# Kernel tuning notes

Hardware: AMD Instinct MI355X
Metric: run time of the kernel (lower is better)

## Reference

```python
import jax, jax.numpy as jnp
import numpy as np
import math

B, H, L, DK, D, LOCAL = 4, 8, 2048, 64, 512, 4


def setup_inputs() -> dict:
    key = jax.random.key(0)
    ks = jax.random.split(key, 9)
    n = L
    return {
        'query': jax.random.normal(ks[0], (B, H, L, DK), jnp.float32),
        'key': jax.random.normal(ks[1], (B, H, L, DK), jnp.float32),
        'value': jax.random.normal(ks[2], (B, H, L, DK), jnp.float32),
        'users': jax.random.normal(ks[3], (B, L, D), jnp.float32),
        'mask': jnp.tril(jnp.ones((L, L), dtype=bool))[None, None],  # causal [1,1,L,L]
        'rel_pos_w': jax.random.normal(ks[4], (2 * n - 1, DK * LOCAL), jnp.float32) * 0.02,
        'user_proj_w': jax.random.normal(ks[5], (DK * LOCAL, D), jnp.float32) * 0.02,
        'user_proj_b': jax.random.normal(ks[6], (DK * LOCAL,), jnp.float32) * 0.02,
        'mlp_w': jax.random.normal(ks[7], (LOCAL, DK), jnp.float32) * 0.1,
        'mlp_b': jax.random.normal(ks[8], (LOCAL,), jnp.float32) * 0.1,
    }


def reference(query, key, value, users, mask, rel_pos_w, user_proj_w, user_proj_b, mlp_w, mlp_b):
    b, h, l, dk = query.shape
    local = mlp_w.shape[0]
    g = h - local
    n = l
    scale = 1.0 / math.sqrt(dk)
    NEG = -1e12  # MAX_VAL in the torch source

    # ---- global heads: plain softmax attention ----
    qg, kg, vg = query[:, :g], key[:, :g], value[:, :g]
    sg = jnp.einsum('bhqd,bhkd->bhqk', qg, kg) * scale
    sg = jnp.where(mask, sg, NEG)
    pg = jax.nn.softmax(sg, axis=-1)
    og = jnp.einsum('bhqk,bhkd->bhqd', pg, vg)

    # ---- local (LOCKER) heads ----
    ql, kl, vl = query[:, g:], key[:, g:], value[:, g:]
    sl = jnp.einsum('bhqd,bhkd->bhqk', ql, kl) * scale

    # reweight = Linear(d_k,1)(rel_pos + v_q + v_k + user_proj(users)_q) per local head.
    # Linear over a sum decomposes exactly (same math, avoids [b,local,l,l,dk] tensor):
    rel_tab = rel_pos_w.reshape(2 * n - 1, local, dk)
    rel_scores = jnp.einsum('rhd,hd->rh', rel_tab, mlp_w)          # [2n-1, local]
    pos = jnp.arange(n)
    distance = pos[None, :] - pos[:, None] + n - 1                  # [l, l]
    rel_term = rel_scores[distance].transpose(2, 0, 1)              # [local, l, l]

    v_term = jnp.einsum('bhkd,hd->bhk', vl, mlp_w)                  # [b, local, l]
    u = (users @ user_proj_w.T + user_proj_b).reshape(b, l, local, dk)
    u_term = jnp.einsum('bqhd,hd->bhq', u, mlp_w)                   # [b, local, l]

    reweight = (rel_term[None]
                + v_term[:, :, None, :]      # value_l.unsqueeze(-3): varies over key idx
                + v_term[:, :, :, None]      # value_l.unsqueeze(-2): varies over query idx
                + u_term[:, :, :, None]      # user term broadcast over key idx
                + mlp_b[None, :, None, None])

    sl = sl + reweight
    sl = jnp.where(mask, sl, NEG)
    pl = jax.nn.softmax(sl, axis=-1)
    ol = jnp.einsum('bhqk,bhkd->bhqd', pl, vl)

    return jnp.concatenate([og, ol], axis=1)  # [b, h, l, d_k]
```

## Files before the change

kernel.cpp:

```cpp
#include <hip/hip_runtime.h>

#define TL 2048
#define NHEAD 8
#define NLOC 4
#define L2E 1.44269504f
#define PSTRIDE 4352

typedef __attribute__((ext_vector_type(4))) float f32x4;
typedef __attribute__((ext_vector_type(16))) float f32x16;
typedef __attribute__((ext_vector_type(8))) __bf16 bf16x8;
typedef __attribute__((ext_vector_type(8))) unsigned short u16x8;
typedef __attribute__((ext_vector_type(4))) unsigned int u32x4;

static __device__ __forceinline__ unsigned short f2bf(float f) {
    unsigned u = __float_as_uint(f);
    u = (u + 0x7FFFu + ((u >> 16) & 1u)) >> 16;
    return (unsigned short)u;
}
static __device__ __forceinline__ unsigned int cvtpk(float a, float b) {
    unsigned int w;
    asm("v_cvt_pk_bf16_f32 %0, %1, %2" : "=v"(w) : "v"(a), "v"(b));
    return w;
}
static __device__ __forceinline__ void gl_lds16(const void* g, void* l) {
    __builtin_amdgcn_global_load_lds(
        (const __attribute__((address_space(1))) void*)g,
        (__attribute__((address_space(3))) void*)l, 16, 0, 0);
}

__global__ __launch_bounds__(256) void relscore_kernel(
    const float* __restrict__ rel_pos_w, const float* __restrict__ mlp_w,
    float* __restrict__ rel_sf) {
    int r = blockIdx.x;
    int t = threadIdx.x;
    int w = t >> 6, lane = t & 63;
    float v = rel_pos_w[r * 256 + t] * mlp_w[t];
#pragma unroll
    for (int off = 32; off; off >>= 1) v += __shfl_xor(v, off);
    if (lane == 0) rel_sf[w * 4096 + r] = v * L2E;
}

__global__ __launch_bounds__(256) void preconv_kernel(
    const float* __restrict__ key, const float* __restrict__ value,
    const float* __restrict__ mlp_w,
    unsigned short* __restrict__ Kb, unsigned short* __restrict__ Vtb,
    float* __restrict__ vtbf) {
    __shared__ float Vf[64][66];
    int blk = blockIdx.x;
    int t = threadIdx.x;
    int bh = blk >> 5, kt = blk & 31;
    int h = bh & 7, b = bh >> 3;
    size_t src = (size_t)blk * 4096;
    size_t dst = (size_t)blk * 4096;

#pragma unroll
    for (int i = 0; i < 2; ++i) {
        int ch = t + i * 256;
        int row = ch >> 3, c = ch & 7;
        const float* kp = key + src + row * 64 + c * 8;
        f32x4 a = *(const f32x4*)kp;
        f32x4 bb = *(const f32x4*)(kp + 4);
        u16x8 o;
#pragma unroll
        for (int j = 0; j < 4; ++j) { o[j] = f2bf(a[j]); o[4 + j] = f2bf(bb[j]); }
        *(u16x8*)&Kb[dst + row * 64 + ((c ^ (row & 7)) << 3)] = o;
    }
    {
        int row = t >> 2, q4 = t & 3;
        const float* vp = value + src + row * 64 + q4 * 16;
#pragma unroll
        for (int j = 0; j < 4; ++j)
            *(f32x4*)&Vf[row][q4 * 16 + j * 4] = *(const f32x4*)(vp + j * 4);
    }
    __syncthreads();
#pragma unroll
    for (int i = 0; i < 2; ++i) {
        int ch = t + i * 256;
        int dr = ch >> 3, c = ch & 7;
        u16x8 o;
#pragma unroll
        for (int j = 0; j < 8; ++j) o[j] = f2bf(Vf[c * 8 + j][dr]);
        *(u16x8*)&Vtb[dst + dr * 64 + ((c ^ (dr & 7)) << 3)] = o;
    }
    if (h >= NLOC) {
        int wave = t >> 6, lane = t & 63;
        float mw = mlp_w[(h - NLOC) * 64 + lane];
        float* vout = vtbf + (size_t)((b * NLOC + h - NLOC) * TL) + kt * 64;
#pragma unroll
        for (int i = 0; i < 16; ++i) {
            int row = wave * 16 + i;
            float v = Vf[row][lane] * mw;
#pragma unroll
            for (int off = 32; off; off >>= 1) v += __shfl_xor(v, off);
            if (lane == 0) vout[row] = v * L2E;
        }
    }
}

#define MFMA32(A, B, C) __builtin_amdgcn_mfma_f32_32x32x16_bf16(A, B, C, 0, 0, 0)

__global__ __launch_bounds__(256, 4) void attn_kernel(
    const float* __restrict__ query,
    const unsigned short* __restrict__ Kb, const unsigned short* __restrict__ Vtb,
    const float* __restrict__ rel_sf, const float* __restrict__ vtbf,
    float* __restrict__ part) {

    __shared__ __align__(16) unsigned char smem[35328];
    unsigned short* Ks0 = (unsigned short*)smem;
    unsigned short* Vt0 = (unsigned short*)(smem + 16384);
    float* relw  = (float*)(smem + 32768);
    float* biasf = (float*)(smem + 34816);

    int bid = blockIdx.x;
    int bh = bid & 31;
    int sid = bid >> 5;
    int i = 0, s = 0, acc = 0;
#pragma unroll
    for (int ii = 15; ii >= 0; --ii) {
        int ns = (2 * ii + 7) / 6;
        if (sid >= acc && sid < acc + ns) { i = ii; s = sid - acc; }
        acc += ns;
    }
    int k_b = 6 * s;
    int k_e = min(6 * s + 6, 2 * i + 2);
    int q0 = i << 7;

    int h = bh & 7, b = bh >> 3;
    bool islocal = (h >= NLOC);
    int t = threadIdx.x;
    int w = t >> 6;
    int l31 = t & 31;
    int hi = (t >> 5) & 1;
    int sw = l31 & 7;
    int qrel = 32 * w + l31;
    int qglob = q0 + qrel;
    int qmaxw = q0 + 32 * w + 31;

    size_t tbase = (size_t)bh * 32 * 4096;
    const unsigned short* Ktiles = Kb + tbase;
    const unsigned short* Vtiles = Vtb + tbase;
    const float* vtpf = vtbf + (islocal ? (size_t)((b * NLOC + h - NLOC) * TL) : 0);
    int idxlo = 64 * k_b - q0 + 1920;
    const float* relsrc = rel_sf + (islocal ? ((h - NLOC) * 4096 + idxlo) : 0);

    gl_lds16(Ktiles + (size_t)k_b * 4096 + t * 8, Ks0 + t * 8);
    gl_lds16(Ktiles + (size_t)k_b * 4096 + 2048 + t * 8, Ks0 + 2048 + t * 8);
    gl_lds16(Vtiles + (size_t)k_b * 4096 + t * 8, Vt0 + t * 8);
    gl_lds16(Vtiles + (size_t)k_b * 4096 + 2048 + t * 8, Vt0 + 2048 + t * 8);
    if (islocal) {
        if (t < 128) *((f32x4*)relw + t) = *((const f32x4*)relsrc + t);
        if (t < 16) ((f32x4*)biasf)[t] = ((const f32x4*)(vtpf + (size_t)k_b * 64))[t];
    }

    const float SC = 0.125f * L2E;
    bf16x8 qf[4];
    {
        const float* qsrc = query + ((size_t)bh * TL + qglob) * 64 + 8 * hi;
#pragma unroll
        for (int mq = 0; mq < 4; ++mq) {
            f32x4 a = *(const f32x4*)(qsrc + 16 * mq);
            f32x4 c = *(const f32x4*)(qsrc + 16 * mq + 4);
            u16x8 u;
#pragma unroll
            for (int j = 0; j < 4; ++j) { u[j] = f2bf(a[j] * SC); u[4 + j] = f2bf(c[j] * SC); }
            qf[mq] = __builtin_bit_cast(bf16x8, u);
        }
    }

    float m = -1e30f, lsum = 0.f;
    f32x16 O0 = {0,0,0,0,0,0,0,0,0,0,0,0,0,0,0,0};
    f32x16 O1 = {0,0,0,0,0,0,0,0,0,0,0,0,0,0,0,0};

    __syncthreads();

    int cur = 0;
    for (int kt = k_b; kt < k_e; ++kt) {
        unsigned short* Ks = Ks0 + cur * 4096;
        unsigned short* Vt = Vt0 + cur * 4096;
        const float* bias = biasf + cur * 64;

        if (kt + 1 < k_e) {
            int nb = cur ^ 1;
            gl_lds16(Ktiles + (size_t)(kt + 1) * 4096 + t * 8, Ks0 + nb * 4096 + t * 8);
            gl_lds16(Ktiles + (size_t)(kt + 1) * 4096 + 2048 + t * 8, Ks0 + nb * 4096 + 2048 + t * 8);
            gl_lds16(Vtiles + (size_t)(kt + 1) * 4096 + t * 8, Vt0 + nb * 4096 + t * 8);
            gl_lds16(Vtiles + (size_t)(kt + 1) * 4096 + 2048 + t * 8, Vt0 + nb * 4096 + 2048 + t * 8);
            if (islocal && t < 16)
                ((f32x4*)(biasf + nb * 64))[t] =
                    ((const f32x4*)(vtpf + (size_t)(kt + 1) * 64))[t];
        }

        bool active = (64 * kt <= qmaxw);
        bool maskt = (64 * kt + 63 > q0 + 32 * w);
        if (active) {
#pragma unroll
            for (int h2 = 0; h2 < 2; ++h2) {
                f32x16 S = {0,0,0,0,0,0,0,0,0,0,0,0,0,0,0,0};
#pragma unroll
                for (int mq = 0; mq < 4; ++mq) {
                    int ch = ((2 * mq + hi) ^ sw) << 3;
                    const bf16x8 kf = *(const bf16x8*)&Ks[(32 * h2 + l31) * 64 + ch];
                    S = MFMA32(kf, qf[mq], S);
                }

                if (islocal) {
                    int rbase = 64 * (kt - k_b) + 32 * h2 + 4 * hi + 127 - qrel;
#pragma unroll
                    for (int g = 0; g < 4; ++g) {
                        int kk0 = 32 * h2 + 8 * g + 4 * hi;
                        f32x4 bv = *(const f32x4*)&bias[kk0];
#pragma unroll
                        for (int j = 0; j < 4; ++j)
                            S[4 * g + j] += bv[j] + relw[rbase + 8 * g + j];
                    }
                }
                if (maskt) {
                    int koff = 64 * kt + 32 * h2 + 4 * hi - qglob;
#pragma unroll
                    for (int r = 0; r < 16; ++r) {
                        int kk = (r & 3) + 8 * (r >> 2);
                        if (koff + kk > 0) S[r] = -1e30f;
                    }
                }
                float pmax = -1e30f;
#pragma unroll
                for (int r = 0; r < 16; ++r) pmax = fmaxf(pmax, S[r]);
                pmax = fmaxf(pmax, __shfl_xor(pmax, 32));
                if (__any(pmax > m + 11.5f)) {
                    float nm2 = fmaxf(m, pmax);
                    float corr = exp2f(m - nm2);
                    lsum *= corr;
#pragma unroll
                    for (int r = 0; r < 16; ++r) { O0[r] *= corr; O1[r] *= corr; }
                    m = nm2;
                }
                float ps = 0.f;
#pragma unroll
                for (int r = 0; r < 16; ++r) {
                    float p = exp2f(S[r] - m);
                    S[r] = p; ps += p;
                }
                ps += __shfl_xor(ps, 32);
                lsum += ps;

#pragma unroll
                for (int kq = 0; kq < 2; ++kq) {
                    int ra = 8 * kq;
                    unsigned int x0 = cvtpk(S[ra + 0], S[ra + 1]);
                    unsigned int x1 = cvtpk(S[ra + 2], S[ra + 3]);
                    unsigned int y0 = cvtpk(S[ra + 4], S[ra + 5]);
                    unsigned int y1 = cvtpk(S[ra + 6], S[ra + 7]);
                    unsigned int sx0 = __shfl_xor(x0, 32), sx1 = __shfl_xor(x1, 32);
                    unsigned int sy0 = __shfl_xor(y0, 32), sy1 = __shfl_xor(y1, 32);
                    u32x4 fw;
                    fw[0] = hi ? sy0 : x0;
                    fw[1] = hi ? sy1 : x1;
                    fw[2] = hi ? y0 : sx0;
                    fw[3] = hi ? y1 : sx1;
                    const bf16x8 pf = __builtin_bit_cast(bf16x8, fw);
                    int ch = ((4 * h2 + 2 * kq + hi) ^ sw) << 3;
                    const bf16x8 vf0 = *(const bf16x8*)&Vt[l31 * 64 + ch];
                    const bf16x8 vf1 = *(const bf16x8*)&Vt[(32 + l31) * 64 + ch];
                    O0 = MFMA32(vf0, pf, O0);
                    O1 = MFMA32(vf1, pf, O1);
                }
            }
        }
        __syncthreads();
        cur ^= 1;
    }

    float* pp = part + (size_t)bid * PSTRIDE;
    unsigned int* po = (unsigned int*)pp;
#pragma unroll
    for (int g = 0; g < 4; ++g) {
        unsigned int w0 = cvtpk(O0[4 * g + 0], O0[4 * g + 1]);
        unsigned int w1 = cvtpk(O0[4 * g + 2], O0[4 * g + 3]);
        unsigned int w2 = cvtpk(O1[4 * g + 0], O1[4 * g + 1]);
        unsigned int w3 = cvtpk(O1[4 * g + 2], O1[4 * g + 3]);
        int dp0 = 4 * g + 2 * hi;
        po[dp0 * 128 + qrel] = w0;
        po[(dp0 + 1) * 128 + qrel] = w1;
        po[(16 + dp0) * 128 + qrel] = w2;
        po[(16 + dp0 + 1) * 128 + qrel] = w3;
    }
    if (hi == 0) { pp[4096 + qrel] = m; pp[4224 + qrel] = lsum; }
}

__global__ __launch_bounds__(128) void merge_kernel(
    const float* __restrict__ part, float* __restrict__ out) {
    __shared__ float sc[6][128];
    int bid = blockIdx.x;
    int bh = bid & 31, i = bid >> 5;
    int n = (2 * i + 7) / 6;
    int sb = 0;
    for (int ii = 15; ii > i; --ii) sb += (2 * ii + 7) / 6;
    int t = threadIdx.x;

    float mv[6], lv[6];
#pragma unroll
    for (int s2 = 0; s2 < 6; ++s2) {
        mv[s2] = -1e30f; lv[s2] = 0.f;
        if (s2 < n) {
            const float* pp = part + (size_t)((sb + s2) * 32 + bh) * PSTRIDE;
            mv[s2] = pp[4096 + t]; lv[s2] = pp[4224 + t];
        }
    }
    float nm = mv[0];
#pragma unroll
    for (int s2 = 1; s2 < 6; ++s2) nm = fmaxf(nm, mv[s2]);
    float den = 0.f;
    float cf[6];
#pragma unroll
    for (int s2 = 0; s2 < 6; ++s2) { cf[s2] = exp2f(mv[s2] - nm); den += lv[s2] * cf[s2]; }
    float inv = 1.0f / den;
#pragma unroll
    for (int s2 = 0; s2 < 6; ++s2) if (s2 < n) sc[s2][t] = cf[s2] * inv;
    __syncthreads();

    size_t obase = (size_t)bh * TL * 64 + (size_t)(128 * i + t) * 64;
    for (int seg = 0; seg < 4; ++seg) {
        float o[16];
#pragma unroll
        for (int j = 0; j < 16; ++j) o[j] = 0.f;
#pragma unroll
        for (int s2 = 0; s2 < 6; ++s2) {
            if (s2 < n) {
                const unsigned int* po =
                    (const unsigned int*)(part + (size_t)((sb + s2) * 32 + bh) * PSTRIDE);
                float wsc = sc[s2][t];
#pragma unroll
                for (int j = 0; j < 8; ++j) {
                    unsigned int wv = po[(seg * 8 + j) * 128 + t];
                    o[2 * j]     += wsc * __uint_as_float((wv & 0xffffu) << 16);
                    o[2 * j + 1] += wsc * __uint_as_float(wv & 0xffff0000u);
                }
            }
        }
#pragma unroll
        for (int c = 0; c < 4; ++c)
            *(f32x4*)(out + obase + seg * 16 + 4 * c) = *(const f32x4*)&o[4 * c];
    }
}

extern "C" void kernel_launch(void* const* d_in, const int* in_sizes, int n_in,
                              void* d_out, int out_size, void* d_ws, size_t ws_size,
                              hipStream_t stream) {
    const float* query = (const float*)d_in[0];
    const float* key = (const float*)d_in[1];
    const float* value = (const float*)d_in[2];
    const float* rel_pos_w = (const float*)d_in[5];
    const float* mlp_w = (const float*)d_in[8];
    float* out = (float*)d_out;

    unsigned short* Kb = (unsigned short*)d_ws;
    unsigned short* Vtb = Kb + 32 * 32 * 4096;
    float* rel_sf = (float*)(Vtb + 32 * 32 * 4096);
    float* vtbf = rel_sf + 4 * 4096;
    float* part = vtbf + 32768;

    relscore_kernel<<<4095, 256, 0, stream>>>(rel_pos_w, mlp_w, rel_sf);
    preconv_kernel<<<1024, 256, 0, stream>>>(key, value, mlp_w, Kb, Vtb, vtbf);
    attn_kernel<<<1632, 256, 0, stream>>>(query, Kb, Vtb, rel_sf, vtbf, part);
    merge_kernel<<<512, 128, 0, stream>>>(part, out);
}
```

Measured before the change: 82.10 us.

## Fuse relscore into preconv, add MFMA priority hints, use permlane32 swap

Folds the relative-position score computation into extra blocks of the preconversion kernel, removing one kernel launch. It also wraps the MFMA sections in s_setprio raises so waves issuing matrix ops get scheduling priority. The P-fragment exchange between half-waves now uses v_permlane32_swap instead of four shuffles plus selects. The swap must reproduce the original lane selection exactly, and the setprio effect depends on how waves interleave.

```diff
diff --git a/kernel.cpp b/kernel.cpp
--- a/kernel.cpp
+++ b/kernel.cpp
@@ -28,26 +28,30 @@
         (__attribute__((address_space(3))) void*)l, 16, 0, 0);
 }
 
-__global__ __launch_bounds__(256) void relscore_kernel(
-    const float* __restrict__ rel_pos_w, const float* __restrict__ mlp_w,
-    float* __restrict__ rel_sf) {
-    int r = blockIdx.x;
-    int t = threadIdx.x;
-    int w = t >> 6, lane = t & 63;
-    float v = rel_pos_w[r * 256 + t] * mlp_w[t];
-#pragma unroll
-    for (int off = 32; off; off >>= 1) v += __shfl_xor(v, off);
-    if (lane == 0) rel_sf[w * 4096 + r] = v * L2E;
-}
-
 __global__ __launch_bounds__(256) void preconv_kernel(
     const float* __restrict__ key, const float* __restrict__ value,
-    const float* __restrict__ mlp_w,
+    const float* __restrict__ mlp_w, const float* __restrict__ rel_pos_w,
     unsigned short* __restrict__ Kb, unsigned short* __restrict__ Vtb,
-    float* __restrict__ vtbf) {
-    __shared__ float Vf[64][66];
+    float* __restrict__ vtbf, float* __restrict__ rel_sf) {
     int blk = blockIdx.x;
     int t = threadIdx.x;
+    int wave = t >> 6, lane = t & 63;
+
+    if (blk >= 1024) {
+        int r = (blk - 1024) * 4 + wave;
+        if (r < 2 * TL - 1) {
+#pragma unroll
+            for (int hp = 0; hp < 4; ++hp) {
+                float v = rel_pos_w[r * 256 + hp * 64 + lane] * mlp_w[hp * 64 + lane];
+#pragma unroll
+                for (int off = 32; off; off >>= 1) v += __shfl_xor(v, off);
+                if (lane == 0) rel_sf[hp * 4096 + r] = v * L2E;
+            }
+        }
+        return;
+    }
+
+    __shared__ float Vf[64][66];
     int bh = blk >> 5, kt = blk & 31;
     int h = bh & 7, b = bh >> 3;
     size_t src = (size_t)blk * 4096;
@@ -83,7 +87,6 @@
         *(u16x8*)&Vtb[dst + dr * 64 + ((c ^ (dr & 7)) << 3)] = o;
     }
     if (h >= NLOC) {
-        int wave = t >> 6, lane = t & 63;
         float mw = mlp_w[(h - NLOC) * 64 + lane];
         float* vout = vtbf + (size_t)((b * NLOC + h - NLOC) * TL) + kt * 64;
 #pragma unroll
@@ -196,12 +199,14 @@
 #pragma unroll
             for (int h2 = 0; h2 < 2; ++h2) {
                 f32x16 S = {0,0,0,0,0,0,0,0,0,0,0,0,0,0,0,0};
+                __builtin_amdgcn_s_setprio(1);
 #pragma unroll
                 for (int mq = 0; mq < 4; ++mq) {
                     int ch = ((2 * mq + hi) ^ sw) << 3;
                     const bf16x8 kf = *(const bf16x8*)&Ks[(32 * h2 + l31) * 64 + ch];
                     S = MFMA32(kf, qf[mq], S);
                 }
+                __builtin_amdgcn_s_setprio(0);
 
                 if (islocal) {
                     int rbase = 64 * (kt - k_b) + 32 * h2 + 4 * hi + 127 - qrel;
@@ -243,6 +248,7 @@
                 ps += __shfl_xor(ps, 32);
                 lsum += ps;
 
+                __builtin_amdgcn_s_setprio(1);
 #pragma unroll
                 for (int kq = 0; kq < 2; ++kq) {
                     int ra = 8 * kq;
@@ -250,13 +256,10 @@
                     unsigned int x1 = cvtpk(S[ra + 2], S[ra + 3]);
                     unsigned int y0 = cvtpk(S[ra + 4], S[ra + 5]);
                     unsigned int y1 = cvtpk(S[ra + 6], S[ra + 7]);
-                    unsigned int sx0 = __shfl_xor(x0, 32), sx1 = __shfl_xor(x1, 32);
-                    unsigned int sy0 = __shfl_xor(y0, 32), sy1 = __shfl_xor(y1, 32);
+                    asm("v_permlane32_swap_b32 %0, %1" : "+v"(x0), "+v"(y0));
+                    asm("v_permlane32_swap_b32 %0, %1" : "+v"(x1), "+v"(y1));
                     u32x4 fw;
-                    fw[0] = hi ? sy0 : x0;
-                    fw[1] = hi ? sy1 : x1;
-                    fw[2] = hi ? y0 : sx0;
-                    fw[3] = hi ? y1 : sx1;
+                    fw[0] = x0; fw[1] = x1; fw[2] = y0; fw[3] = y1;
                     const bf16x8 pf = __builtin_bit_cast(bf16x8, fw);
                     int ch = ((4 * h2 + 2 * kq + hi) ^ sw) << 3;
                     const bf16x8 vf0 = *(const bf16x8*)&Vt[l31 * 64 + ch];
@@ -264,6 +267,7 @@
                     O0 = MFMA32(vf0, pf, O0);
                     O1 = MFMA32(vf1, pf, O1);
                 }
+                __builtin_amdgcn_s_setprio(0);
             }
         }
         __syncthreads();
@@ -359,8 +363,8 @@
     float* vtbf = rel_sf + 4 * 4096;
     float* part = vtbf + 32768;
 
-    relscore_kernel<<<4095, 256, 0, stream>>>(rel_pos_w, mlp_w, rel_sf);
-    preconv_kernel<<<1024, 256, 0, stream>>>(key, value, mlp_w, Kb, Vtb, vtbf);
+    preconv_kernel<<<2048, 256, 0, stream>>>(key, value, mlp_w, rel_pos_w,
+                                             Kb, Vtb, vtbf, rel_sf);
     attn_kernel<<<1632, 256, 0, stream>>>(query, Kb, Vtb, rel_sf, vtbf, part);
     merge_kernel<<<512, 128, 0, stream>>>(part, out);
 }
```

Result: faster. 75.57 us (-7.9%).
